# Optimization experiments

Hardware: AMD Instinct MI355X
Metric: run time of the kernel (lower is better)

The kernel has to match this reference:

```python
import jax, jax.numpy as jnp
import numpy as np

SIZE = 256
R = 896          # total radial bins = nodes per sample (128 + 4*64 + 16*32)
LMAX = 510       # widest folded ring row (i=127 -> 4i+2)
WMAX = LMAX - 1  # conv output width (kernel=2)
HID = 32         # ConvAutoEncoder hidden channels (create_layers default)
ENC = 10         # hidden_encoder (per-bin embedding dim)
GCN_H = 64
NCLS = 10
B = 8
EPS = 7168       # edges per sample (avg degree 8)
PAD = 3 * SIZE * SIZE  # padding gather index -> zero column


def _reshape_2d(arr, border):
    # verbatim port of reshape_2d, applied to index arrays
    ptr_st, ptr_end = border, len(arr) - border
    d1 = list(arr[:ptr_st]); d2 = list(arr[ptr_end:])
    itt = 4
    while ptr_st != ptr_end:
        (d1 if itt > 2 else d2).append(arr[ptr_st])
        ptr_st += 1; itt -= 1
        if itt == 0:
            itt = 4
    return np.stack([d1, d2])


def build_static():
    # For each radial bin rad in 0..895: flat gather indices (into the
    # concatenated 3*256*256 per-sample maps) in boolean-mask (row-major)
    # order, folded by reshape_2d to (2, 4i+2), padded to LMAX with PAD.
    idx = np.full((R, 2, LMAX), PAD, np.int32)
    band = np.zeros(R, np.int32)
    rad = 0
    for m, coef in enumerate([1, 2, 4]):
        step = SIZE // coef
        c = step / 2 - 0.5
        ii, jj = np.meshgrid(np.arange(step), np.arange(step), indexing='ij')
        d = (np.maximum(np.abs(ii - c), np.abs(jj - c)) // 1).astype(int)  # create_circular
        for by in range(coef):
            for bx in range(coef):
                flat = m * SIZE * SIZE + (by * step + ii) * SIZE + (bx * step + jj)
                for i in range(step // 2):
                    sel = flat[d == i]                    # row-major ring pixels (8i+4)
                    two = _reshape_2d(sel, 2 + 2 * i)     # (2, 4i+2)
                    L = two.shape[1]
                    idx[rad, :, :L] = two
                    band[rad] = L - 1                     # band_length = 4i+1
                    rad += 1
    return idx, band


def gcn_conv(x, W, b, src, dst, ew, n):
    # torch_geometric GCNConv: add self loops (w=1), symmetric norm, aggregate at dst
    loop = jnp.arange(n)
    s = jnp.concatenate([src, loop])
    t = jnp.concatenate([dst, loop])
    w = jnp.concatenate([ew, jnp.ones((n,), x.dtype)])
    deg = jax.ops.segment_sum(w, t, num_segments=n)
    dinv = jnp.where(deg > 0, jax.lax.rsqrt(jnp.maximum(deg, 1e-12)), 0.0)
    norm = dinv[s] * w * dinv[t]
    xw = x @ W
    return jax.ops.segment_sum(norm[:, None] * xw[s], t, num_segments=n) + b


def setup_inputs() -> dict:
    key = jax.random.key(0)
    ks = jax.random.split(key, 12)
    idx_np, band = build_static()
    x = jax.random.normal(ks[0], (B, 3, SIZE, SIZE), jnp.float32)
    base = jax.random.randint(ks[1], (2, B, EPS), 0, R)
    edge_index = (base + (jnp.arange(B) * R)[None, :, None]).reshape(2, -1)
    batch_vec = jnp.arange(B * R, dtype=jnp.int32) // R
    Wconv = jax.random.normal(ks[2], (R, HID, 2, 2), jnp.float32) * 0.3
    bconv = jax.random.normal(ks[3], (R, HID), jnp.float32) * 0.05
    # decoder padded to WMAX, zeroed beyond each bin's band length (exact math)
    mask = (np.arange(WMAX)[None, :] < band[:, None]).astype(np.float32)
    Wdec = jax.random.normal(ks[4], (R, ENC, HID, WMAX), jnp.float32) * 0.02
    Wdec = Wdec * jnp.asarray(mask)[:, None, None, :]
    bdec = jax.random.normal(ks[5], (R, ENC), jnp.float32) * 0.05
    edge_w = jax.random.normal(ks[6], (EPS,), jnp.float32)
    Wg1 = jax.random.normal(ks[7], (ENC, GCN_H), jnp.float32) * (1.0 / np.sqrt(ENC))
    bg1 = jnp.zeros((GCN_H,), jnp.float32)
    Wg2 = jax.random.normal(ks[8], (GCN_H, GCN_H), jnp.float32) * (1.0 / np.sqrt(GCN_H))
    bg2 = jnp.zeros((GCN_H,), jnp.float32)
    Wl = jax.random.normal(ks[9], (GCN_H, NCLS), jnp.float32) * (1.0 / np.sqrt(GCN_H))
    bl = jnp.zeros((NCLS,), jnp.float32)
    return dict(x=x, edge_index=edge_index, batch_vec=batch_vec, idx=jnp.asarray(idx_np),
                Wconv=Wconv, bconv=bconv, Wdec=Wdec, bdec=bdec, edge_w=edge_w,
                Wg1=Wg1, bg1=bg1, Wg2=Wg2, bg2=bg2, Wl=Wl, bl=bl)


def reference(x, edge_index, batch_vec, idx, Wconv, bconv, Wdec, bdec, edge_w,
              Wg1, bg1, Wg2, bg2, Wl, bl):
    b = x.shape[0]
    n = b * R
    # --- get_embedding: batched radial-bin gather + per-bin 2x2 conv + linear ---
    xp = jnp.concatenate([x.reshape(b, -1), jnp.zeros((b, 1), x.dtype)], axis=1)
    vals = xp[:, idx]                                         # (B,R,2,LMAX)
    win = jnp.stack([vals[..., :-1], vals[..., 1:]], axis=-1)  # (B,R,2,WMAX,2) = b r kh w kw
    h = jax.nn.relu(jnp.einsum('brhwk,rchk->brcw', win, Wconv) + bconv[:, :, None])
    emb = jnp.einsum('brcw,rocw->bro', h, Wdec) + bdec         # (B,R,ENC)
    nodes = emb.reshape(n, ENC)
    # --- GCN: trainable sigmoid edge weights tiled per sample ---
    ew = jax.nn.sigmoid(jnp.tile(edge_w, b))
    src, dst = edge_index[0], edge_index[1]
    h1 = jax.nn.relu(gcn_conv(nodes, Wg1, bg1, src, dst, ew, n))
    h2 = gcn_conv(h1, Wg2, bg2, src, dst, ew, n)
    pooled = jax.ops.segment_sum(h2, batch_vec, num_segments=b) / R  # global_mean_pool (equal sizes)
    # dropout p=0.1 in eval mode -> identity
    return jax.nn.softmax(pooled @ Wl + bl, axis=1)
```

## Files before the change

### kernel.cpp

```cpp
#include <hip/hip_runtime.h>

static constexpr int kR    = 896;
static constexpr int kLMAX = 510;
static constexpr int kWMAX = 509;
static constexpr int kHID  = 32;
static constexpr int kENC  = 10;
static constexpr int kGH   = 64;
static constexpr int kNCLS = 10;
static constexpr int kB    = 8;
static constexpr int kEPS  = 7168;
static constexpr int kN    = kB * kR;
static constexpr int kE    = kB * kEPS;
static constexpr int kPAD  = 3 * 256 * 256;

constexpr int band_of(int r) {
    int i = (r < 128) ? r : (r < 384) ? ((r - 128) & 63) : ((r - 384) & 31);
    return 4 * i + 1;
}
__device__ __forceinline__ int band_dev(int r) {
    int i = (r < 128) ? r : (r < 384) ? ((r - 128) & 63) : ((r - 384) & 31);
    return 4 * i + 1;
}

static constexpr int kCHUNK = 256;
constexpr int count_chunks() {
    int n = 0;
    for (int r = 0; r < kR; ++r) n += (band_of(r) + kCHUNK - 1) / kCHUNK;
    return n;
}
static constexpr int kNCHUNK = count_chunks();
static_assert(kNCHUNK == 960, "chunk count");

struct CE { short r; short w0; };
struct Tab { CE e[kNCHUNK]; };
constexpr Tab make_tab() {
    Tab t{};
    int n = 0;
    for (int pass = 0; pass < 2; ++pass) {
        for (int r = 0; r < kR; ++r) {
            const int bnd = band_of(r);
            for (int w0 = 0; w0 < bnd; w0 += kCHUNK) {
                int wc = bnd - w0; if (wc > kCHUNK) wc = kCHUNK;
                const bool wide = (wc >= 128);
                if ((pass == 0) == wide) { t.e[n].r = (short)r; t.e[n].w0 = (short)w0; ++n; }
            }
        }
    }
    return t;
}
__device__ __constant__ Tab g_tab = make_tab();

static constexpr size_t OFF_EMB  = 0;
static constexpr size_t OFF_DEG  = OFF_EMB + 71680;
static constexpr size_t OFF_CNT  = OFF_DEG + 7168;
static constexpr size_t OFF_POOL = OFF_CNT + 7168;
static constexpr size_t kMEMSET_FLOATS = OFF_POOL + 512;
static constexpr size_t OFF_DINV = kMEMSET_FLOATS;
static constexpr size_t OFF_CSUM = OFF_DINV + 7168;
static constexpr size_t OFF_OFFS = OFF_CSUM + 7168;
static constexpr size_t OFF_WOFF = OFF_OFFS + 7169;
static constexpr size_t OFF_CSRC = OFF_WOFF + 7169;
static constexpr size_t OFF_CNRM = OFF_CSRC + 57344;
static constexpr size_t OFF_XW1  = OFF_CNRM + 57344;
static constexpr size_t OFF_XT   = (OFF_XW1 + 458752 + 7) & ~(size_t)7;

__device__ __forceinline__ float sigmoidf_(float v) { return 1.0f / (1.0f + expf(-v)); }

__global__ __launch_bounds__(256)
void k_xpose(const float* __restrict__ x, const int* __restrict__ ei,
             const float* __restrict__ edge_w,
             float* __restrict__ xt, float* __restrict__ deg, int* __restrict__ cnt)
{
    const int bid = blockIdx.x;
    const int tid = threadIdx.x;
    if (bid < kPAD / 256) {
        const int j = bid * 256 + tid;
        float4 lo, hi;
        lo.x = x[(size_t)0 * kPAD + j]; lo.y = x[(size_t)1 * kPAD + j];
        lo.z = x[(size_t)2 * kPAD + j]; lo.w = x[(size_t)3 * kPAD + j];
        hi.x = x[(size_t)4 * kPAD + j]; hi.y = x[(size_t)5 * kPAD + j];
        hi.z = x[(size_t)6 * kPAD + j]; hi.w = x[(size_t)7 * kPAD + j];
        float4* dst = (float4*)&xt[(size_t)j * 8];
        dst[0] = lo; dst[1] = hi;
    } else {
        const int e = (bid - kPAD / 256) * 256 + tid;
        if (e < kE) {
            const int t = ei[kE + e];
            atomicAdd(&deg[t], sigmoidf_(edge_w[e % kEPS]));
            atomicAdd(&cnt[t], 1);
        }
    }
}

__global__ __launch_bounds__(320)
void k_conv_emb(const float* __restrict__ xt, const int* __restrict__ idx,
                const float* __restrict__ Wconv, const float* __restrict__ bconv,
                const float* __restrict__ Wdec, float* __restrict__ emb)
{
    const int bid = blockIdx.x;
    const int tid = threadIdx.x;

    const int r     = g_tab.e[bid].r;
    const int w0    = g_tab.e[bid].w0;
    const int bandr = band_dev(r);
    const int wc    = min(kCHUNK, bandr - w0);

    __shared__ float vals[2][kB][kCHUNK + 1];
    __shared__ float wconv_s[kHID * 4];
    __shared__ float bconv_s[kHID];

    if (tid < 128) wconv_s[tid] = Wconv[r * 128 + tid];
    else if (tid < 160) bconv_s[tid - 128] = bconv[r * kHID + (tid - 128)];

    for (int i = tid; i < 2 * (kCHUNK + 1); i += 320) {
        const int hh = i >= (kCHUNK + 1);
        const int li = i - hh * (kCHUNK + 1);
        const int j = (li <= wc) ? idx[(r * 2 + hh) * kLMAX + w0 + li] : kPAD;
        float4 lo = {0, 0, 0, 0}, hi = {0, 0, 0, 0};
        if ((unsigned)j < (unsigned)kPAD) {
            const float4* src = (const float4*)&xt[(size_t)j * 8];
            lo = src[0]; hi = src[1];
        }
        vals[hh][0][li] = lo.x; vals[hh][1][li] = lo.y;
        vals[hh][2][li] = lo.z; vals[hh][3][li] = lo.w;
        vals[hh][4][li] = hi.x; vals[hh][5][li] = hi.y;
        vals[hh][6][li] = hi.z; vals[hh][7][li] = hi.w;
    }
    __syncthreads();

    const int wave = tid >> 6, lane = tid & 63;
    const int o0 = wave * 2;
    const float* Wd0 = Wdec + ((size_t)(r * kENC + o0) * kHID) * kWMAX;
    const float* Wd1 = Wd0 + (size_t)kHID * kWMAX;

    float acc0[8] = {0,0,0,0,0,0,0,0}, acc1[8] = {0,0,0,0,0,0,0,0};

    #pragma unroll 1
    for (int st = 0; st < kCHUNK / 64; ++st) {
        if (st * 64 >= wc) break;
        const int wl = st * 64 + lane;
        const bool valid = (wl < wc);
        const int w = w0 + wl;

        float v00[8], v01[8], v10[8], v11[8];
        #pragma unroll
        for (int b = 0; b < 8; ++b) {
            v00[b] = vals[0][b][wl]; v01[b] = vals[0][b][wl + 1];
            v10[b] = vals[1][b][wl]; v11[b] = vals[1][b][wl + 1];
        }

        #pragma unroll 8
        for (int c = 0; c < kHID; ++c) {
            const float wd0 = valid ? Wd0[(size_t)c * kWMAX + w] : 0.0f;
            const float wd1 = valid ? Wd1[(size_t)c * kWMAX + w] : 0.0f;
            const float w00 = wconv_s[c * 4 + 0], w01 = wconv_s[c * 4 + 1];
            const float w10 = wconv_s[c * 4 + 2], w11 = wconv_s[c * 4 + 3];
            const float bc  = bconv_s[c];
            #pragma unroll
            for (int b = 0; b < 8; ++b) {
                float h = fmaf(v00[b], w00, fmaf(v01[b], w01,
                          fmaf(v10[b], w10, fmaf(v11[b], w11, bc))));
                h = fmaxf(h, 0.0f);
                acc0[b] = fmaf(wd0, h, acc0[b]);
                acc1[b] = fmaf(wd1, h, acc1[b]);
            }
        }
    }

    #pragma unroll
    for (int b = 0; b < 8; ++b) {
        float s0 = acc0[b], s1 = acc1[b];
        #pragma unroll
        for (int sft = 32; sft > 0; sft >>= 1) {
            s0 += __shfl_xor(s0, sft);
            s1 += __shfl_xor(s1, sft);
        }
        if (lane == 0) {
            atomicAdd(&emb[((size_t)b * kR + r) * kENC + o0],     s0);
            atomicAdd(&emb[((size_t)b * kR + r) * kENC + o0 + 1], s1);
        }
    }
}

__global__ __launch_bounds__(256)
void k_scanxw1(const float* __restrict__ deg, const int* __restrict__ cnt,
               float* __restrict__ dinv, float* __restrict__ colsum,
               int* __restrict__ off, int* __restrict__ woff,
               const float* __restrict__ emb, const float* __restrict__ bdec,
               const float* __restrict__ Wg1, float* __restrict__ xw1)
{
    const int bid = blockIdx.x;
    const int t = threadIdx.x;
    if (bid > 0) {
        const int tt = (bid - 1) * 256 + t;
        const int i = tt >> 6, f = tt & 63;
        const int r = i % kR;
        float s = 0.0f;
        #pragma unroll
        for (int o = 0; o < kENC; ++o)
            s = fmaf(emb[i * kENC + o] + bdec[r * kENC + o], Wg1[o * kGH + f], s);
        xw1[tt] = s;
        return;
    }

    for (int i = t; i < kN; i += 256) {
        float d = deg[i] + 1.0f;
        dinv[i]   = rsqrtf(d);
        colsum[i] = 1.0f / d;
    }
    __shared__ int cl[kN];
    for (int i = t; i < kN; i += 256) cl[i] = cnt[i];
    __syncthreads();

    int loc[28];
    int s = 0;
    const int base = t * 28;
    #pragma unroll
    for (int k = 0; k < 28; ++k) { loc[k] = s; s += cl[base + k]; }

    __shared__ int sa[256], sb[256];
    sa[t] = s;
    __syncthreads();
    int* in = sa; int* out = sb;
    for (int d = 1; d < 256; d <<= 1) {
        out[t] = in[t] + ((t >= d) ? in[t - d] : 0);
        __syncthreads();
        int* tmp = in; in = out; out = tmp;
    }
    const int incl = in[t];
    const int excl = incl - s;
    #pragma unroll
    for (int k = 0; k < 28; ++k) {
        off[base + k]  = excl + loc[k];
        woff[base + k] = excl + loc[k];
    }
    if (t == 255) off[kN] = incl;
}

__global__ __launch_bounds__(256)
void k_fill(const int* __restrict__ ei, const float* __restrict__ edge_w,
            const float* __restrict__ dinv, int* __restrict__ woff,
            int* __restrict__ csrc, float* __restrict__ cnrm,
            float* __restrict__ colsum)
{
    int e = blockIdx.x * 256 + threadIdx.x;
    if (e >= kE) return;
    const int s = ei[e], t = ei[kE + e];
    const float nm = dinv[s] * sigmoidf_(edge_w[e % kEPS]) * dinv[t];
    const int p = atomicAdd(&woff[t], 1);
    csrc[p] = s;
    cnrm[p] = nm;
    atomicAdd(&colsum[s], nm);
}

__global__ __launch_bounds__(256)
void k_agg(const float* __restrict__ xw1, const int* __restrict__ off,
           const int* __restrict__ csrc, const float* __restrict__ cnrm,
           const float* __restrict__ dinv, const float* __restrict__ colsum,
           const float* __restrict__ bg1, const float* __restrict__ Wg2,
           float* __restrict__ pooled)
{
    const int tid  = threadIdx.x;
    const int wave = tid >> 6, f = tid & 63;

    __shared__ float wg2s[kGH * kGH];
    __shared__ float hrow[4][kGH];
    __shared__ float pool_s[kGH];

    for (int i = tid; i < kGH * kGH; i += 256) wg2s[i] = Wg2[i];
    if (tid < kGH) pool_s[tid] = 0.0f;
    __syncthreads();

    const int j0 = blockIdx.x * 16;
    #pragma unroll
    for (int q = 0; q < 4; ++q) {
        const int j = j0 + wave * 4 + q;
        const float di = dinv[j];
        float a = fmaf(di * di, xw1[(size_t)j * kGH + f], bg1[f]);
        const int pb = off[j], pe = off[j + 1];
        int   sC = 0; float nC = 0.0f;
        if (pb < pe) { sC = csrc[pb]; nC = cnrm[pb]; }
        for (int p = pb; p < pe; ++p) {
            int sN = sC; float nN = 0.0f;
            if (p + 1 < pe) { sN = csrc[p + 1]; nN = cnrm[p + 1]; }
            a = fmaf(nC, xw1[(size_t)sC * kGH + f], a);
            sC = sN; nC = nN;
        }
        a = fmaxf(a, 0.0f);
        hrow[wave][f] = a;
        float s2 = 0.0f;
        #pragma unroll 8
        for (int f2 = 0; f2 < kGH; ++f2)
            s2 = fmaf(hrow[wave][f2], wg2s[f2 * kGH + f], s2);
        atomicAdd(&pool_s[f], colsum[j] * s2);
    }
    __syncthreads();
    if (tid < kGH) {
        const int b = j0 / kR;
        atomicAdd(&pooled[b * kGH + tid], pool_s[tid]);
    }
}

__global__ __launch_bounds__(128)
void k_head(const float* __restrict__ pooled, const float* __restrict__ bg2,
            const float* __restrict__ Wl, const float* __restrict__ bl,
            float* __restrict__ out)
{
    const int t = threadIdx.x;
    __shared__ float lgs[kB * kNCLS];
    if (t < kB * kNCLS) {
        const int b = t / kNCLS, c = t % kNCLS;
        float s = bl[c];
        for (int g = 0; g < kGH; ++g) {
            const float pg = bg2[g] + pooled[b * kGH + g] * (1.0f / kR);
            s = fmaf(pg, Wl[g * kNCLS + c], s);
        }
        lgs[t] = s;
    }
    __syncthreads();
    if (t < kB) {
        float mx = lgs[t * kNCLS];
        for (int j = 1; j < kNCLS; ++j) mx = fmaxf(mx, lgs[t * kNCLS + j]);
        float ssum = 0.0f, ex[kNCLS];
        for (int j = 0; j < kNCLS; ++j) { ex[j] = expf(lgs[t * kNCLS + j] - mx); ssum += ex[j]; }
        for (int j = 0; j < kNCLS; ++j) out[t * kNCLS + j] = ex[j] / ssum;
    }
}

extern "C" void kernel_launch(void* const* d_in, const int* in_sizes, int n_in,
                              void* d_out, int out_size, void* d_ws, size_t ws_size,
                              hipStream_t stream)
{
    const float* x      = (const float*)d_in[0];
    const int*   ei     = (const int*)d_in[1];
    const int*   idx    = (const int*)d_in[3];
    const float* Wconv  = (const float*)d_in[4];
    const float* bconv  = (const float*)d_in[5];
    const float* Wdec   = (const float*)d_in[6];
    const float* bdec   = (const float*)d_in[7];
    const float* edge_w = (const float*)d_in[8];
    const float* Wg1    = (const float*)d_in[9];
    const float* bg1    = (const float*)d_in[10];
    const float* Wg2    = (const float*)d_in[11];
    const float* bg2    = (const float*)d_in[12];
    const float* Wl     = (const float*)d_in[13];
    const float* bl     = (const float*)d_in[14];

    float* ws     = (float*)d_ws;
    float* emb    = ws + OFF_EMB;
    float* deg    = ws + OFF_DEG;
    int*   cnt    = (int*)(ws + OFF_CNT);
    float* pooled = ws + OFF_POOL;
    float* dinv   = ws + OFF_DINV;
    float* colsum = ws + OFF_CSUM;
    int*   off    = (int*)(ws + OFF_OFFS);
    int*   woff   = (int*)(ws + OFF_WOFF);
    int*   csrc   = (int*)(ws + OFF_CSRC);
    float* cnrm   = ws + OFF_CNRM;
    float* xw1    = ws + OFF_XW1;
    float* xt     = ws + OFF_XT;

    hipMemsetAsync(ws, 0, kMEMSET_FLOATS * sizeof(float), stream);

    k_xpose<<<kPAD / 256 + (kE + 255) / 256, 256, 0, stream>>>(x, ei, edge_w, xt, deg, cnt);

    k_conv_emb<<<kNCHUNK, 320, 0, stream>>>(xt, idx, Wconv, bconv, Wdec, emb);

    k_scanxw1<<<1 + kN * kGH / 256, 256, 0, stream>>>(deg, cnt, dinv, colsum, off, woff,
                                                      emb, bdec, Wg1, xw1);
    k_fill<<<(kE + 255) / 256, 256, 0, stream>>>(ei, edge_w, dinv, woff, csrc, cnrm, colsum);
    k_agg <<<kN / 16, 256, 0, stream>>>(xw1, off, csrc, cnrm, dinv, colsum, bg1, Wg2, pooled);
    k_head<<<1, 128, 0, stream>>>(pooled, bg2, Wl, bl, (float*)d_out);
}
```

Measured before the change: 122.1 us.

## Stream decoder weights into LDS with double-buffered async loads, halve chunk size

```diff
diff --git a/kernel.cpp b/kernel.cpp
--- a/kernel.cpp
+++ b/kernel.cpp
@@ -22,14 +22,14 @@
     return 4 * i + 1;
 }
 
-static constexpr int kCHUNK = 256;
+static constexpr int kCHUNK = 128;
 constexpr int count_chunks() {
     int n = 0;
     for (int r = 0; r < kR; ++r) n += (band_of(r) + kCHUNK - 1) / kCHUNK;
     return n;
 }
 static constexpr int kNCHUNK = count_chunks();
-static_assert(kNCHUNK == 960, "chunk count");
+static_assert(kNCHUNK == 1216, "chunk count");
 
 struct CE { short r; short w0; };
 struct Tab { CE e[kNCHUNK]; };
@@ -108,13 +108,14 @@
     __shared__ float vals[2][kB][kCHUNK + 1];
     __shared__ float wconv_s[kHID * 4];
     __shared__ float bconv_s[kHID];
+    __shared__ float wbuf[5][2][8][kCHUNK];
 
     if (tid < 128) wconv_s[tid] = Wconv[r * 128 + tid];
     else if (tid < 160) bconv_s[tid - 128] = bconv[r * kHID + (tid - 128)];
 
-    for (int i = tid; i < 2 * (kCHUNK + 1); i += 320) {
-        const int hh = i >= (kCHUNK + 1);
-        const int li = i - hh * (kCHUNK + 1);
+    if (tid < 2 * (kCHUNK + 1)) {
+        const int hh = tid >= (kCHUNK + 1);
+        const int li = tid - hh * (kCHUNK + 1);
         const int j = (li <= wc) ? idx[(r * 2 + hh) * kLMAX + w0 + li] : kPAD;
         float4 lo = {0, 0, 0, 0}, hi = {0, 0, 0, 0};
         if ((unsigned)j < (unsigned)kPAD) {
@@ -126,43 +127,76 @@
         vals[hh][4][li] = hi.x; vals[hh][5][li] = hi.y;
         vals[hh][6][li] = hi.z; vals[hh][7][li] = hi.w;
     }
-    __syncthreads();
 
     const int wave = tid >> 6, lane = tid & 63;
     const int o0 = wave * 2;
-    const float* Wd0 = Wdec + ((size_t)(r * kENC + o0) * kHID) * kWMAX;
-    const float* Wd1 = Wd0 + (size_t)kHID * kWMAX;
+    const float* WdR = Wdec + (size_t)(r * kENC) * kHID * kWMAX;
+    const int lhalf = lane >> 5;
+    const int lwf   = (lane & 31) * 4;
+
+    auto stage = [&](int g) {
+        const int cq = g * 4;
+        const int d = g & 1;
+        #pragma unroll
+        for (int j = 0; j < 4; ++j) {
+            const int o = (j < 2) ? o0 : (o0 + 1);
+            const int cbase = cq + (j & 1) * 2;
+            const float* gp = WdR + ((size_t)(o * kHID + cbase + lhalf)) * kWMAX + w0 + lwf;
+            float* lp = &wbuf[wave][d][j * 2][0];
+            __builtin_amdgcn_global_load_lds(
+                (const __attribute__((address_space(1))) unsigned int*)(const void*)gp,
+                (__attribute__((address_space(3))) unsigned int*)(void*)lp, 16, 0, 0);
+        }
+    };
+
+    stage(0);
+    __syncthreads();
+
+    float v00a[8], v01a[8], v10a[8], v11a[8];
+    float v00b[8], v01b[8], v10b[8], v11b[8];
+    #pragma unroll
+    for (int b = 0; b < 8; ++b) {
+        v00a[b] = vals[0][b][lane];          v01a[b] = vals[0][b][lane + 1];
+        v10a[b] = vals[1][b][lane];          v11a[b] = vals[1][b][lane + 1];
+        v00b[b] = vals[0][b][64 + lane];     v01b[b] = vals[0][b][64 + lane + 1];
+        v10b[b] = vals[1][b][64 + lane];     v11b[b] = vals[1][b][64 + lane + 1];
+    }
+    const bool va = (lane < wc);
+    const bool vb = (64 + lane < wc);
 
     float acc0[8] = {0,0,0,0,0,0,0,0}, acc1[8] = {0,0,0,0,0,0,0,0};
 
     #pragma unroll 1
-    for (int st = 0; st < kCHUNK / 64; ++st) {
-        if (st * 64 >= wc) break;
-        const int wl = st * 64 + lane;
-        const bool valid = (wl < wc);
-        const int w = w0 + wl;
-
-        float v00[8], v01[8], v10[8], v11[8];
+    for (int g = 0; g < 8; ++g) {
+        if (g < 7) {
+            stage(g + 1);
+            asm volatile("s_waitcnt vmcnt(4)" ::: "memory");
+        } else {
+            asm volatile("s_waitcnt vmcnt(0)" ::: "memory");
+        }
+        __builtin_amdgcn_sched_barrier(0);
+        const int d = g & 1;
+        const int cq = g * 4;
         #pragma unroll
-        for (int b = 0; b < 8; ++b) {
-            v00[b] = vals[0][b][wl]; v01[b] = vals[0][b][wl + 1];
-            v10[b] = vals[1][b][wl]; v11[b] = vals[1][b][wl + 1];
-        }
-
-        #pragma unroll 8
-        for (int c = 0; c < kHID; ++c) {
-            const float wd0 = valid ? Wd0[(size_t)c * kWMAX + w] : 0.0f;
-            const float wd1 = valid ? Wd1[(size_t)c * kWMAX + w] : 0.0f;
+        for (int cc = 0; cc < 4; ++cc) {
+            const int c = cq + cc;
             const float w00 = wconv_s[c * 4 + 0], w01 = wconv_s[c * 4 + 1];
             const float w10 = wconv_s[c * 4 + 2], w11 = wconv_s[c * 4 + 3];
             const float bc  = bconv_s[c];
+            const float wd0a = va ? wbuf[wave][d][cc][lane] : 0.0f;
+            const float wd0b = vb ? wbuf[wave][d][cc][64 + lane] : 0.0f;
+            const float wd1a = va ? wbuf[wave][d][4 + cc][lane] : 0.0f;
+            const float wd1b = vb ? wbuf[wave][d][4 + cc][64 + lane] : 0.0f;
             #pragma unroll
             for (int b = 0; b < 8; ++b) {
-                float h = fmaf(v00[b], w00, fmaf(v01[b], w01,
-                          fmaf(v10[b], w10, fmaf(v11[b], w11, bc))));
-                h = fmaxf(h, 0.0f);
-                acc0[b] = fmaf(wd0, h, acc0[b]);
-                acc1[b] = fmaf(wd1, h, acc1[b]);
+                float ha = fmaf(v00a[b], w00, fmaf(v01a[b], w01,
+                           fmaf(v10a[b], w10, fmaf(v11a[b], w11, bc))));
+                ha = fmaxf(ha, 0.0f);
+                float hb = fmaf(v00b[b], w00, fmaf(v01b[b], w01,
+                           fmaf(v10b[b], w10, fmaf(v11b[b], w11, bc))));
+                hb = fmaxf(hb, 0.0f);
+                acc0[b] = fmaf(wd0a, ha, fmaf(wd0b, hb, acc0[b]));
+                acc1[b] = fmaf(wd1a, ha, fmaf(wd1b, hb, acc1[b]));
             }
         }
     }
```

Result: slower. 150.3 us (+23.1%).
